# Kernel optimization log

Hardware: AMD Instinct MI355X
Metric: run time of the kernel (lower is better)

## Reference

```python
import math
import jax, jax.numpy as jnp
import numpy as np


def setup_inputs() -> dict:
    B, MA, ME = 512, 64, 256
    d_model, d_qk, N = 256, 32, 200000
    rng = np.random.default_rng(0)
    actor_len = rng.integers(1, MA + 1, B)
    actee_len = rng.integers(1, ME + 1, B)
    # flat scatter positions: indices(1) + indices(0) * max_len
    qindices = np.concatenate([np.arange(l) + i * MA for i, l in enumerate(actor_len)]).astype(np.int64)
    kindices = np.concatenate([np.arange(l) + i * ME for i, l in enumerate(actee_len)]).astype(np.int64)
    A, E = len(qindices), len(kindices)
    actors = rng.integers(0, N, A)            # absolute indices into x (offsets pre-applied)
    actees = rng.integers(0, N, E)
    # previous action for each actor must index a valid actee of its env
    prev_actions = rng.integers(0, np.repeat(actee_len, actor_len))
    key = jax.random.key(0)
    k0, k1, k2 = jax.random.split(key, 3)
    s = 1.0 / math.sqrt(d_model)
    return {
        "x": jax.random.normal(k0, (N, d_model), jnp.float32),
        "Wq": jax.random.normal(k1, (d_model, d_qk), jnp.float32) * s,
        "bq": jnp.zeros((d_qk,), jnp.float32),
        "Wk": jax.random.normal(k2, (d_model, d_qk), jnp.float32) * s,
        "bk": jnp.zeros((d_qk,), jnp.float32),
        "actors": jnp.asarray(actors, jnp.int32),
        "qindices": jnp.asarray(qindices, jnp.int32),
        "actees": jnp.asarray(actees, jnp.int32),
        "kindices": jnp.asarray(kindices, jnp.int32),
        "prev_actions": jnp.asarray(prev_actions, jnp.int32),
        "B": B, "max_actors": MA, "max_actees": ME,
    }


def reference(x, Wq, bq, Wk, bk, actors, qindices, actees, kindices, prev_actions, B, max_actors, max_actees):
    d_qk = Wq.shape[1]
    scale = 1.0 / math.sqrt(d_qk)
    queries = x[actors] @ Wq + bq                         # [A, d_qk] ragged gather + project
    keys = x[actees] @ Wk + bk                            # [E, d_qk]
    # scatter into zero-padded (queries) / one-padded (keys) buffers
    pq = jnp.zeros((B * max_actors, d_qk), x.dtype).at[qindices].set(queries).reshape(B, max_actors, d_qk)
    qmask = jnp.zeros((B * max_actors,), x.dtype).at[qindices].set(1.0).reshape(B, max_actors)
    pk = jnp.ones((B * max_actees, d_qk), x.dtype).at[kindices].set(keys).reshape(B, max_actees, d_qk)
    kmask = jnp.zeros((B * max_actees,), x.dtype).at[kindices].set(1.0).reshape(B, max_actees)
    logits = jnp.einsum("bqd,bkd->bqk", pq, pk) * scale   # [B, max_actors, max_actees]
    valid = qmask[:, :, None] * kmask[:, None, :]
    logits = jnp.where(valid == 0, jnp.asarray(-1e9, x.dtype), logits)
    # prev_actions branch: scatter actions into one-padded buffer
    padded_actions = jnp.ones((B * max_actors,), jnp.int32).at[qindices].set(prev_actions).reshape(B, max_actors)
    logp = jax.nn.log_softmax(logits, axis=-1)
    logprob = jnp.take_along_axis(logp, padded_actions[:, :, None], axis=-1)[..., 0]  # [B, max_actors]
    entropy = -jnp.sum(jnp.exp(logp) * logp, axis=-1)
    # gather-back to ragged layout
    return (
        padded_actions.reshape(-1)[qindices],
        logprob.reshape(-1)[qindices],
        entropy.reshape(-1)[qindices],
        logits,
    )
```

## Files before the change

### kernel.cpp

```cpp
#include <hip/hip_runtime.h>
#include <math.h>

#define MA 64
#define ME 256
#define DM 256
#define DQK 32
#define ENVSTRIDE (MA * ME)
#define MASKVAL -998244352.0f
#define QK_SCALE 0.17677669529663687f
#define KSTR 40

typedef __attribute__((ext_vector_type(8))) short bf16x8;
typedef __attribute__((ext_vector_type(4))) float f32x4;
typedef unsigned short u16;

__device__ __forceinline__ int lb(const int* __restrict__ a, int n, int v){
  int lo = 0, hi = n;
  while (lo < hi){ int mid = (lo + hi) >> 1; if (a[mid] < v) lo = mid + 1; else hi = mid; }
  return lo;
}
__device__ __forceinline__ unsigned pk2bf(float lo, float hi){
  unsigned ul = __float_as_uint(lo); ul = ul + 0x7FFFu + ((ul >> 16) & 1u);
  unsigned uh = __float_as_uint(hi); uh = uh + 0x7FFFu + ((uh >> 16) & 1u);
  return (ul >> 16) | (uh & 0xFFFF0000u);
}
__device__ __forceinline__ u16 f2bu(float f){
  unsigned u = __float_as_uint(f);
  return (u16)((u + 0x7FFFu + ((u >> 16) & 1u)) >> 16);
}

__global__ __launch_bounds__(256)
void pack_w(const float* __restrict__ Wk, const float* __restrict__ Wq,
            unsigned* __restrict__ wfr_g){
  const int base = blockIdx.x * 512 + threadIdx.x;
  #pragma unroll
  for (int ii = 0; ii < 2; ++ii) {
    const int i = base + ii * 256;
    const int p = i & 3, ln = (i >> 2) & 63, nt = (i >> 8) & 1, kk = (i >> 9) & 7, wh = i >> 12;
    const int k0  = kk * 32 + (ln >> 4) * 8 + 2 * p;
    const int col = nt * 16 + (ln & 15);
    const float* W = wh ? Wq : Wk;
    wfr_g[i] = pk2bf(W[(size_t)k0 * DQK + col], W[(size_t)(k0 + 1) * DQK + col]);
  }
}

__global__ __launch_bounds__(256)
void fused_env(const float* __restrict__ x,
               const float* __restrict__ bq, const float* __restrict__ bk,
               const int* __restrict__ actors, const int* __restrict__ qindices,
               const int* __restrict__ actees, const int* __restrict__ kindices,
               const int* __restrict__ prev_actions,
               const unsigned* __restrict__ wfr_g,
               int A, int E, float* __restrict__ out)
{
  __shared__ u16 kb[ME * KSTR];
  __shared__ u16 qsm[MA * KSTR];
  __shared__ int srange[4];

  const int t = threadIdx.x, b = blockIdx.x;
  if (t < 4) {
    const int* arr = (t < 2) ? qindices : kindices;
    const int nn = (t < 2) ? A : E;
    const int vv = (t == 0) ? b * MA : (t == 1) ? (b + 1) * MA
                 : (t == 2) ? b * ME : (b + 1) * ME;
    srange[t] = lb(arr, nn, vv);
  }
  __syncthreads();

  const int qstart = srange[0], qlen = srange[1] - srange[0];
  const int kstart = srange[2], klen = srange[3] - srange[2];

  const int lane = t & 63, w = t >> 6;
  const int lr = lane & 15, lq = lane >> 4;

  const float bkv0 = bk[lr], bkv1 = bk[16 + lr];
  const float bqv0 = bq[lr], bqv1 = bq[16 + lr];

  const int kt = (klen + 15) >> 4;
  const int qt = (qlen + 15) >> 4;
  const int ntiles = kt + qt;

  for (int i = w; i < ntiles; i += 4) {
    const bool isk = (i < kt);
    const int  rbase = isk ? (i << 4) : ((i - kt) << 4);
    const int  len   = isk ? klen : qlen;
    const int  start = isk ? kstart : qstart;
    const int* gath  = isk ? actees : actors;
    u16*       dst   = isk ? kb : qsm;
    const unsigned* fb = wfr_g + (isk ? 0 : 4096) + lane * 4;

    bf16x8 bfr[8][2];
    #pragma unroll
    for (int kk = 0; kk < 8; ++kk) {
      bfr[kk][0] = *(const bf16x8*)(fb + kk * 512);
      bfr[kk][1] = *(const bf16x8*)(fb + kk * 512 + 256);
    }

    const int arow = start + min(rbase + lr, len - 1);
    const float* xr = x + (size_t)gath[arow] * DM + lq * 8;

    float4 cx[16];
    #pragma unroll
    for (int kk = 0; kk < 8; ++kk) {
      cx[2*kk]   = *(const float4*)(xr + kk * 32);
      cx[2*kk+1] = *(const float4*)(xr + kk * 32 + 4);
    }

    const float v0 = isk ? bkv0 : bqv0, v1 = isk ? bkv1 : bqv1;
    f32x4 a0 = {v0, v0, v0, v0}, a1 = {v1, v1, v1, v1};
    #pragma unroll
    for (int kk = 0; kk < 8; ++kk) {
      union { unsigned u[4]; bf16x8 v; } fa;
      fa.u[0] = pk2bf(cx[2*kk].x,   cx[2*kk].y);
      fa.u[1] = pk2bf(cx[2*kk].z,   cx[2*kk].w);
      fa.u[2] = pk2bf(cx[2*kk+1].x, cx[2*kk+1].y);
      fa.u[3] = pk2bf(cx[2*kk+1].z, cx[2*kk+1].w);
      a0 = __builtin_amdgcn_mfma_f32_16x16x32_bf16(fa.v, bfr[kk][0], a0, 0, 0, 0);
      a1 = __builtin_amdgcn_mfma_f32_16x16x32_bf16(fa.v, bfr[kk][1], a1, 0, 0, 0);
    }
    #pragma unroll
    for (int reg = 0; reg < 4; ++reg) {
      const int row = rbase + 4 * lq + reg;
      if (row < len) {
        dst[row * KSTR + lr]      = f2bu(a0[reg]);
        dst[row * KSTR + 16 + lr] = f2bu(a1[reg]);
      }
    }
  }
  __syncthreads();

  float* out_lg = out + (size_t)3 * A + (size_t)b * ENVSTRIDE;
  const int row0 = 16 * w;

  if (row0 >= qlen) {
    const float4 mv = make_float4(MASKVAL, MASKVAL, MASKVAL, MASKVAL);
    float4* o4 = (float4*)out_lg;
    #pragma unroll
    for (int rr = 0; rr < 16; ++rr) o4[(row0 + rr) * 64 + lane] = mv;
    return;
  }

  const bf16x8 afr = *(const bf16x8*)&qsm[(row0 + lr) * KSTR + lq * 8];
  f32x4 acc[16];
  #pragma unroll
  for (int nt = 0; nt < 16; ++nt) {
    const bf16x8 bfr2 = *(const bf16x8*)&kb[(16 * nt + lr) * KSTR + lq * 8];
    f32x4 z = {0.f, 0.f, 0.f, 0.f};
    acc[nt] = __builtin_amdgcn_mfma_f32_16x16x32_bf16(afr, bfr2, z, 0, 0, 0);
  }

  int par[4];
  float m[4], spa[4], es[4], ts[4];
  #pragma unroll
  for (int reg = 0; reg < 4; ++reg) {
    const int r = row0 + 4 * lq + reg;
    par[reg] = (r < qlen) ? (prev_actions[qstart + r] & (ME - 1)) : -1;
    m[reg] = MASKVAL; spa[reg] = MASKVAL; es[reg] = 0.f; ts[reg] = 0.f;
  }

  #pragma unroll
  for (int nt = 0; nt < 16; ++nt) {
    const int col = 16 * nt + lr;
    const bool kv = (col < klen);
    #pragma unroll
    for (int reg = 0; reg < 4; ++reg) {
      const float d = kv ? acc[nt][reg] * QK_SCALE : MASKVAL;
      acc[nt][reg] = d;
      m[reg] = fmaxf(m[reg], d);
      if (col == par[reg]) spa[reg] = d;
    }
  }
  #pragma unroll
  for (int off = 1; off < 16; off <<= 1) {
    #pragma unroll
    for (int reg = 0; reg < 4; ++reg) {
      m[reg]   = fmaxf(m[reg],   __shfl_xor(m[reg],   off));
      spa[reg] = fmaxf(spa[reg], __shfl_xor(spa[reg], off));
    }
  }
  #pragma unroll
  for (int nt = 0; nt < 16; ++nt) {
    #pragma unroll
    for (int reg = 0; reg < 4; ++reg) {
      const float dd = acc[nt][reg] - m[reg];
      if (dd > -80.f) { const float e = __expf(dd); es[reg] += e; ts[reg] += e * dd; }
    }
  }
  #pragma unroll
  for (int off = 1; off < 16; off <<= 1) {
    #pragma unroll
    for (int reg = 0; reg < 4; ++reg) {
      es[reg] += __shfl_xor(es[reg], off);
      ts[reg] += __shfl_xor(ts[reg], off);
    }
  }

  #pragma unroll
  for (int nt = 0; nt < 16; ++nt) {
    #pragma unroll
    for (int reg = 0; reg < 4; ++reg) {
      const int r = row0 + 4 * lq + reg;
      out_lg[r * ME + 16 * nt + lr] = (r < qlen) ? acc[nt][reg] : MASKVAL;
    }
  }
  if (lr == 0) {
    #pragma unroll
    for (int reg = 0; reg < 4; ++reg) {
      const int r = row0 + 4 * lq + reg;
      if (r < qlen) {
        const float lS = __logf(fmaxf(es[reg], 1e-30f));
        out[qstart + r]         = (float)par[reg];
        out[A + qstart + r]     = spa[reg] - m[reg] - lS;
        out[2 * A + qstart + r] = lS - ts[reg] / es[reg];
      }
    }
  }
}

extern "C" void kernel_launch(void* const* d_in, const int* in_sizes, int n_in,
                              void* d_out, int out_size, void* d_ws, size_t ws_size,
                              hipStream_t stream) {
  const float* x  = (const float*)d_in[0];
  const float* Wq = (const float*)d_in[1];
  const float* bq = (const float*)d_in[2];
  const float* Wk = (const float*)d_in[3];
  const float* bk = (const float*)d_in[4];
  const int* actors       = (const int*)d_in[5];
  const int* qindices     = (const int*)d_in[6];
  const int* actees       = (const int*)d_in[7];
  const int* kindices     = (const int*)d_in[8];
  const int* prev_actions = (const int*)d_in[9];

  const int A = in_sizes[5];
  const int E = in_sizes[7];
  const int B = (out_size - 3 * A) / ENVSTRIDE;
  if (B <= 0) return;

  unsigned* wfr_g = (unsigned*)d_ws;

  pack_w<<<dim3(16), dim3(256), 0, stream>>>(Wk, Wq, wfr_g);
  fused_env<<<dim3(B), dim3(256), 0, stream>>>(
      x, bq, bk, actors, qindices, actees, kindices, prev_actions,
      wfr_g, A, E, (float*)d_out);
}
```

Measured before the change: 45.01 us.

## Precompute env ranges in a separate kernel, stage weights in LDS, prefetch gather indices

Moves the per-block binary searches over qindices/kindices into a small pre-kernel that writes int4 ranges to workspace, which removes the serial search and extra barrier at the start of each block. The packed projection weights are copied once into shared memory rather than reloaded from global memory on every tile. All gather indices for up to five tiles per wave are loaded ahead of the barrier so the row loads can be issued sooner. This adds a kernel launch and about 32KB more LDS per block, which may lower occupancy, and it assumes at most 5 tiles per wave.

```diff
diff --git a/kernel.cpp b/kernel.cpp
--- a/kernel.cpp
+++ b/kernel.cpp
@@ -29,6 +29,17 @@
   return (u16)((u + 0x7FFFu + ((u >> 16) & 1u)) >> 16);
 }
 
+__global__ void ranges_kernel(const int* __restrict__ qindices, const int* __restrict__ kindices,
+                              int A, int E, int B, int4* __restrict__ rng){
+  int e = blockIdx.x * blockDim.x + threadIdx.x;
+  if (e >= B) return;
+  int qs = lb(qindices, A, e * MA);
+  int qe = lb(qindices, A, e * MA + MA);
+  int ks = lb(kindices, E, e * ME);
+  int ke = lb(kindices, E, e * ME + ME);
+  rng[e] = make_int4(qs, qe - qs, ks, ke - ks);
+}
+
 __global__ __launch_bounds__(256)
 void pack_w(const float* __restrict__ Wk, const float* __restrict__ Wq,
             unsigned* __restrict__ wfr_g){
@@ -50,28 +61,26 @@
                const int* __restrict__ actors, const int* __restrict__ qindices,
                const int* __restrict__ actees, const int* __restrict__ kindices,
                const int* __restrict__ prev_actions,
-               const unsigned* __restrict__ wfr_g,
+               const unsigned* __restrict__ wfr_g, const int4* __restrict__ rng,
                int A, int E, float* __restrict__ out)
 {
+  __shared__ __align__(16) unsigned wfr32[2 * 8 * 2 * 256];
   __shared__ u16 kb[ME * KSTR];
   __shared__ u16 qsm[MA * KSTR];
-  __shared__ int srange[4];
 
   const int t = threadIdx.x, b = blockIdx.x;
-  if (t < 4) {
-    const int* arr = (t < 2) ? qindices : kindices;
-    const int nn = (t < 2) ? A : E;
-    const int vv = (t == 0) ? b * MA : (t == 1) ? (b + 1) * MA
-                 : (t == 2) ? b * ME : (b + 1) * ME;
-    srange[t] = lb(arr, nn, vv);
-  }
-  __syncthreads();
-
-  const int qstart = srange[0], qlen = srange[1] - srange[0];
-  const int kstart = srange[2], klen = srange[3] - srange[2];
-
   const int lane = t & 63, w = t >> 6;
   const int lr = lane & 15, lq = lane >> 4;
+
+  const int4 rg = rng[b];
+  const int qstart = rg.x, qlen = rg.y, kstart = rg.z, klen = rg.w;
+
+  {
+    const float4* src = (const float4*)wfr_g;
+    float4* dst = (float4*)wfr32;
+    #pragma unroll
+    for (int ii = 0; ii < 8; ++ii) dst[t + ii * 256] = src[t + ii * 256];
+  }
 
   const float bkv0 = bk[lr], bkv1 = bk[16 + lr];
   const float bqv0 = bq[lr], bqv1 = bq[16 + lr];
@@ -79,51 +88,61 @@
   const int kt = (klen + 15) >> 4;
   const int qt = (qlen + 15) >> 4;
   const int ntiles = kt + qt;
-
-  for (int i = w; i < ntiles; i += 4) {
-    const bool isk = (i < kt);
-    const int  rbase = isk ? (i << 4) : ((i - kt) << 4);
-    const int  len   = isk ? klen : qlen;
-    const int  start = isk ? kstart : qstart;
-    const int* gath  = isk ? actees : actors;
-    u16*       dst   = isk ? kb : qsm;
-    const unsigned* fb = wfr_g + (isk ? 0 : 4096) + lane * 4;
-
-    bf16x8 bfr[8][2];
-    #pragma unroll
-    for (int kk = 0; kk < 8; ++kk) {
-      bfr[kk][0] = *(const bf16x8*)(fb + kk * 512);
-      bfr[kk][1] = *(const bf16x8*)(fb + kk * 512 + 256);
-    }
-
-    const int arow = start + min(rbase + lr, len - 1);
-    const float* xr = x + (size_t)gath[arow] * DM + lq * 8;
-
-    float4 cx[16];
-    #pragma unroll
-    for (int kk = 0; kk < 8; ++kk) {
-      cx[2*kk]   = *(const float4*)(xr + kk * 32);
-      cx[2*kk+1] = *(const float4*)(xr + kk * 32 + 4);
-    }
-
-    const float v0 = isk ? bkv0 : bqv0, v1 = isk ? bkv1 : bqv1;
-    f32x4 a0 = {v0, v0, v0, v0}, a1 = {v1, v1, v1, v1};
-    #pragma unroll
-    for (int kk = 0; kk < 8; ++kk) {
-      union { unsigned u[4]; bf16x8 v; } fa;
-      fa.u[0] = pk2bf(cx[2*kk].x,   cx[2*kk].y);
-      fa.u[1] = pk2bf(cx[2*kk].z,   cx[2*kk].w);
-      fa.u[2] = pk2bf(cx[2*kk+1].x, cx[2*kk+1].y);
-      fa.u[3] = pk2bf(cx[2*kk+1].z, cx[2*kk+1].w);
-      a0 = __builtin_amdgcn_mfma_f32_16x16x32_bf16(fa.v, bfr[kk][0], a0, 0, 0, 0);
-      a1 = __builtin_amdgcn_mfma_f32_16x16x32_bf16(fa.v, bfr[kk][1], a1, 0, 0, 0);
-    }
-    #pragma unroll
-    for (int reg = 0; reg < 4; ++reg) {
-      const int row = rbase + 4 * lq + reg;
-      if (row < len) {
-        dst[row * KSTR + lr]      = f2bu(a0[reg]);
-        dst[row * KSTR + 16 + lr] = f2bu(a1[reg]);
+  const int nw = (ntiles > w) ? ((ntiles - w + 3) >> 2) : 0;
+
+  int idxv[5];
+  #pragma unroll
+  for (int tt = 0; tt < 5; ++tt) {
+    const int ic = min(w + 4 * tt, ntiles - 1);
+    const bool isk = ic < kt;
+    const int rbase = (isk ? ic : ic - kt) << 4;
+    const int len   = isk ? klen : qlen;
+    const int start = isk ? kstart : qstart;
+    const int* gi   = isk ? actees : actors;
+    idxv[tt] = gi[start + min(rbase + lr, len - 1)];
+  }
+
+  __syncthreads();
+
+  #pragma unroll
+  for (int tt = 0; tt < 5; ++tt) {
+    if (tt < nw) {
+      const int i = w + 4 * tt;
+      const bool isk = (i < kt);
+      const int  rbase = isk ? (i << 4) : ((i - kt) << 4);
+      const int  len   = isk ? klen : qlen;
+      u16*       dst   = isk ? kb : qsm;
+      const unsigned* fb = wfr32 + (isk ? 0 : 4096) + lane * 4;
+
+      const float* xr = x + (size_t)idxv[tt] * DM + lq * 8;
+      float4 cx[16];
+      #pragma unroll
+      for (int kk = 0; kk < 8; ++kk) {
+        cx[2*kk]   = *(const float4*)(xr + kk * 32);
+        cx[2*kk+1] = *(const float4*)(xr + kk * 32 + 4);
+      }
+
+      const float v0 = isk ? bkv0 : bqv0, v1 = isk ? bkv1 : bqv1;
+      f32x4 a0 = {v0, v0, v0, v0}, a1 = {v1, v1, v1, v1};
+      #pragma unroll
+      for (int kk = 0; kk < 8; ++kk) {
+        union { unsigned u[4]; bf16x8 v; } fa;
+        fa.u[0] = pk2bf(cx[2*kk].x,   cx[2*kk].y);
+        fa.u[1] = pk2bf(cx[2*kk].z,   cx[2*kk].w);
+        fa.u[2] = pk2bf(cx[2*kk+1].x, cx[2*kk+1].y);
+        fa.u[3] = pk2bf(cx[2*kk+1].z, cx[2*kk+1].w);
+        const bf16x8 b0 = *(const bf16x8*)(fb + kk * 512);
+        const bf16x8 b1 = *(const bf16x8*)(fb + kk * 512 + 256);
+        a0 = __builtin_amdgcn_mfma_f32_16x16x32_bf16(fa.v, b0, a0, 0, 0, 0);
+        a1 = __builtin_amdgcn_mfma_f32_16x16x32_bf16(fa.v, b1, a1, 0, 0, 0);
+      }
+      #pragma unroll
+      for (int reg = 0; reg < 4; ++reg) {
+        const int row = rbase + 4 * lq + reg;
+        if (row < len) {
+          dst[row * KSTR + lr]      = f2bu(a0[reg]);
+          dst[row * KSTR + 16 + lr] = f2bu(a1[reg]);
+        }
       }
     }
   }
@@ -237,9 +256,11 @@
   if (B <= 0) return;
 
   unsigned* wfr_g = (unsigned*)d_ws;
-
+  int4* rng = (int4*)((char*)d_ws + 32768);
+
+  ranges_kernel<<<dim3((B + 255) / 256), dim3(256), 0, stream>>>(qindices, kindices, A, E, B, rng);
   pack_w<<<dim3(16), dim3(256), 0, stream>>>(Wk, Wq, wfr_g);
   fused_env<<<dim3(B), dim3(256), 0, stream>>>(
       x, bq, bk, actors, qindices, actees, kindices, prev_actions,
-      wfr_g, A, E, (float*)d_out);
-}
+      wfr_g, rng, A, E, (float*)d_out);
+}
```

New measurement: 52.48 us. 1.17x slower.

## Hoist weight fragments out of tile loop and prefetch next gather index

Applied to the files above, without the earlier changes.

The projection loop now loads the packed weight fragments and bias once per wave, reloading only when the wave moves from key tiles to query tiles. It prefetches the next tile's gather index one iteration ahead so the dependent x-row load does not wait on an index load. The x-row load is split into two halves to cut live registers, and launch bounds request 4 blocks per SM for higher occupancy. The trade-off is more control logic, plus a register cap that could cause spills.

```diff
diff --git a/kernel.cpp b/kernel.cpp
--- a/kernel.cpp
+++ b/kernel.cpp
@@ -44,7 +44,7 @@
   }
 }
 
-__global__ __launch_bounds__(256)
+__global__ __launch_bounds__(256, 4)
 void fused_env(const float* __restrict__ x,
                const float* __restrict__ bq, const float* __restrict__ bk,
                const int* __restrict__ actors, const int* __restrict__ qindices,
@@ -73,50 +73,84 @@
   const int lane = t & 63, w = t >> 6;
   const int lr = lane & 15, lq = lane >> 4;
 
-  const float bkv0 = bk[lr], bkv1 = bk[16 + lr];
-  const float bqv0 = bq[lr], bqv1 = bq[16 + lr];
-
   const int kt = (klen + 15) >> 4;
   const int qt = (qlen + 15) >> 4;
   const int ntiles = kt + qt;
 
-  for (int i = w; i < ntiles; i += 4) {
-    const bool isk = (i < kt);
-    const int  rbase = isk ? (i << 4) : ((i - kt) << 4);
-    const int  len   = isk ? klen : qlen;
-    const int  start = isk ? kstart : qstart;
-    const int* gath  = isk ? actees : actors;
-    u16*       dst   = isk ? kb : qsm;
-    const unsigned* fb = wfr_g + (isk ? 0 : 4096) + lane * 4;
-
-    bf16x8 bfr[8][2];
+  bf16x8 bfr[8][2];
+  float bv0, bv1;
+  bool qLoaded = (w >= kt);
+  {
+    const unsigned* fb = wfr_g + (qLoaded ? 4096 : 0) + lane * 4;
     #pragma unroll
     for (int kk = 0; kk < 8; ++kk) {
       bfr[kk][0] = *(const bf16x8*)(fb + kk * 512);
       bfr[kk][1] = *(const bf16x8*)(fb + kk * 512 + 256);
     }
-
-    const int arow = start + min(rbase + lr, len - 1);
-    const float* xr = x + (size_t)gath[arow] * DM + lq * 8;
-
-    float4 cx[16];
-    #pragma unroll
-    for (int kk = 0; kk < 8; ++kk) {
-      cx[2*kk]   = *(const float4*)(xr + kk * 32);
-      cx[2*kk+1] = *(const float4*)(xr + kk * 32 + 4);
-    }
-
-    const float v0 = isk ? bkv0 : bqv0, v1 = isk ? bkv1 : bqv1;
-    f32x4 a0 = {v0, v0, v0, v0}, a1 = {v1, v1, v1, v1};
-    #pragma unroll
-    for (int kk = 0; kk < 8; ++kk) {
-      union { unsigned u[4]; bf16x8 v; } fa;
-      fa.u[0] = pk2bf(cx[2*kk].x,   cx[2*kk].y);
-      fa.u[1] = pk2bf(cx[2*kk].z,   cx[2*kk].w);
-      fa.u[2] = pk2bf(cx[2*kk+1].x, cx[2*kk+1].y);
-      fa.u[3] = pk2bf(cx[2*kk+1].z, cx[2*kk+1].w);
-      a0 = __builtin_amdgcn_mfma_f32_16x16x32_bf16(fa.v, bfr[kk][0], a0, 0, 0, 0);
-      a1 = __builtin_amdgcn_mfma_f32_16x16x32_bf16(fa.v, bfr[kk][1], a1, 0, 0, 0);
+    bv0 = qLoaded ? bq[lr]      : bk[lr];
+    bv1 = qLoaded ? bq[16 + lr] : bk[16 + lr];
+  }
+
+  int idxCur = 0;
+  if (w < ntiles) {
+    const bool isk = w < kt;
+    const int rbase = (isk ? w : w - kt) << 4;
+    const int len   = isk ? klen : qlen;
+    const int* gi   = isk ? actees : actors;
+    const int start = isk ? kstart : qstart;
+    idxCur = gi[start + min(rbase + lr, len - 1)];
+  }
+
+  for (int i = w; i < ntiles; i += 4) {
+    const bool isk = (i < kt);
+    int idxNext = 0;
+    {
+      const int inext = i + 4;
+      if (inext < ntiles) {
+        const bool nk = inext < kt;
+        const int nrb = (nk ? inext : inext - kt) << 4;
+        const int nlen = nk ? klen : qlen;
+        const int* gi  = nk ? actees : actors;
+        const int nst  = nk ? kstart : qstart;
+        idxNext = gi[nst + min(nrb + lr, nlen - 1)];
+      }
+    }
+    if (!isk && !qLoaded) {
+      const unsigned* fb = wfr_g + 4096 + lane * 4;
+      #pragma unroll
+      for (int kk = 0; kk < 8; ++kk) {
+        bfr[kk][0] = *(const bf16x8*)(fb + kk * 512);
+        bfr[kk][1] = *(const bf16x8*)(fb + kk * 512 + 256);
+      }
+      bv0 = bq[lr]; bv1 = bq[16 + lr];
+      qLoaded = true;
+    }
+
+    const int rbase = (isk ? i : i - kt) << 4;
+    const int len   = isk ? klen : qlen;
+    u16* dst        = isk ? kb : qsm;
+    const float* xr = x + (size_t)idxCur * DM + lq * 8;
+
+    f32x4 a0 = {bv0, bv0, bv0, bv0}, a1 = {bv1, bv1, bv1, bv1};
+    #pragma unroll
+    for (int h = 0; h < 2; ++h) {
+      float4 cx[8];
+      #pragma unroll
+      for (int k2 = 0; k2 < 4; ++k2) {
+        cx[2*k2]   = *(const float4*)(xr + h * 128 + k2 * 32);
+        cx[2*k2+1] = *(const float4*)(xr + h * 128 + k2 * 32 + 4);
+      }
+      #pragma unroll
+      for (int k2 = 0; k2 < 4; ++k2) {
+        const int kk = h * 4 + k2;
+        union { unsigned u[4]; bf16x8 v; } fa;
+        fa.u[0] = pk2bf(cx[2*k2].x,   cx[2*k2].y);
+        fa.u[1] = pk2bf(cx[2*k2].z,   cx[2*k2].w);
+        fa.u[2] = pk2bf(cx[2*k2+1].x, cx[2*k2+1].y);
+        fa.u[3] = pk2bf(cx[2*k2+1].z, cx[2*k2+1].w);
+        a0 = __builtin_amdgcn_mfma_f32_16x16x32_bf16(fa.v, bfr[kk][0], a0, 0, 0, 0);
+        a1 = __builtin_amdgcn_mfma_f32_16x16x32_bf16(fa.v, bfr[kk][1], a1, 0, 0, 0);
+      }
     }
     #pragma unroll
     for (int reg = 0; reg < 4; ++reg) {
@@ -126,6 +160,7 @@
         dst[row * KSTR + 16 + lr] = f2bu(a1[reg]);
       }
     }
+    idxCur = idxNext;
   }
   __syncthreads();
 
```

Measured after the change: 45.58 us. Within noise of the previous version (+1.3%).
